# Kernel optimization log

Hardware: AMD Instinct MI355X
Metric: run time of the kernel (lower is better)

## Reference

```python
import jax, jax.numpy as jnp
import numpy as np

H, D = 8, 16          # heads, per-head dim (hidden=128)
N_NEWS, N_INTER, F_IN, C_OUT = 30000, 60000, 768, 4
HID = H * D


def setup_inputs() -> dict:
    key = jax.random.key(0)
    ks = jax.random.split(key, 20)
    s = lambda i, shape, sc=0.05: (jax.random.normal(ks[i], shape, dtype=jnp.float32) * sc)
    inp = {
        "x_news": jax.random.normal(ks[0], (N_NEWS, F_IN), dtype=jnp.float32),
        "x_inter": jax.random.normal(ks[1], (N_INTER, F_IN), dtype=jnp.float32),
        "edge_nn": jax.random.randint(ks[2], (2, 480000), 0, N_NEWS),
        "edge_in": jax.random.randint(ks[3], (2, 960000), 0, N_NEWS),
        # per-node-type input projections (HANConv.proj)
        "W_news": s(4, (F_IN, HID)), "b_news": jnp.zeros((HID,), jnp.float32),
        "W_inter": s(5, (F_IN, HID)), "b_inter": jnp.zeros((HID,), jnp.float32),
        # per-edge-type node-level attention vectors (lin_src / lin_dst)
        "a_src_nn": s(6, (H, D), 0.2), "a_dst_nn": s(7, (H, D), 0.2),
        "a_src_in": s(8, (H, D), 0.2), "a_dst_in": s(9, (H, D), 0.2),
        # semantic-level attention (k_lin, q)
        "Wk": s(10, (HID, HID)), "bk": jnp.zeros((HID,), jnp.float32),
        "q": s(11, (HID,), 0.2),
        # output head
        "W_out": s(12, (HID, C_OUT)), "b_out": jnp.zeros((C_OUT,), jnp.float32),
    }
    return inp


def _han_conv(h_src, h_dst, edge, a_src, a_dst, n_dst):
    # node-level (GAT-style) attention for one edge type
    asrc = (h_src * a_src).sum(-1)            # [Ns, H]
    adst = (h_dst * a_dst).sum(-1)            # [Nd, H]
    src, dst = edge[0], edge[1]
    e = jax.nn.leaky_relu(asrc[src] + adst[dst], negative_slope=0.2)   # [E, H]
    m = jax.ops.segment_max(e, dst, num_segments=n_dst)                # [Nd, H]
    m = jnp.where(jnp.isfinite(m), m, jnp.float32(0))
    ex = jnp.exp(e - m[dst])
    denom = jax.ops.segment_sum(ex, dst, num_segments=n_dst)
    alpha = ex / (denom[dst] + jnp.float32(1e-16))                     # [E, H]
    out = jax.ops.segment_sum(h_src[src] * alpha[:, :, None], dst, num_segments=n_dst)
    return jax.nn.relu(out.reshape(n_dst, H * D))                      # [Nd, HID]


def reference(x_news, x_inter, edge_nn, edge_in,
              W_news, b_news, W_inter, b_inter,
              a_src_nn, a_dst_nn, a_src_in, a_dst_in,
              Wk, bk, q, W_out, b_out):
    # per-node-type projection, reshape to heads
    h_news = (x_news @ W_news + b_news).reshape(-1, H, D)
    h_inter = (x_inter @ W_inter + b_inter).reshape(-1, H, D)
    # per-edge-type node-level attention conv (dst is always 'news')
    out_nn = _han_conv(h_news, h_news, edge_nn, a_src_nn, a_dst_nn, N_NEWS)
    out_in = _han_conv(h_inter, h_news, edge_in, a_src_in, a_dst_in, N_NEWS)
    # semantic-level attention across metapaths
    outs = jnp.stack([out_nn, out_in])                       # [2, N, HID]
    score = (q * jnp.tanh(outs @ Wk + bk).mean(axis=1)).sum(-1)   # [2]
    beta = jax.nn.softmax(score, axis=0)
    fused = (beta[:, None, None] * outs).sum(0)              # [N, HID]
    # head: ELU + (eval-mode dropout = identity) + Linear
    return jax.nn.elu(fused) @ W_out + b_out
```

## Files before the change

kernel.cpp:

```cpp
#include <hip/hip_runtime.h>
#include <hip/hip_bf16.h>

#define N_NODES   30000
#define F_IN      768
#define HID       128
#define NHEAD     8
#define C_OUT     4

typedef short short8_t __attribute__((ext_vector_type(8)));
typedef float float4_t __attribute__((ext_vector_type(4)));
typedef int   int4_t   __attribute__((ext_vector_type(4)));

__device__ __forceinline__ float b2f(short u) {
    union { unsigned int i; float f; } v;
    v.i = ((unsigned int)(unsigned short)u) << 16;
    return v.f;
}
__device__ __forceinline__ short f2s(float f) {
    __hip_bfloat16 h = __float2bfloat16(f);
    short s; __builtin_memcpy(&s, &h, 2); return s;
}

#define OFF_H_NEWS      0UL
#define OFF_H_INTER     7680000UL
#define OFF_OUT_NN      15360000UL
#define OFF_OUT_IN      23040000UL
#define OFF_ASRC_NN     30720000UL
#define OFF_ADST_NN     31680000UL
#define OFF_ASRC_IN     32640000UL
#define OFF_ADST_IN     33600000UL
#define OFF_WT_NEWS     34560000UL
#define OFF_WT_INTER    34756608UL
#define OFF_RS_NN       34953216UL
#define OFF_RS_IN       35073280UL
#define OFF_SORT_NN     35193344UL
#define OFF_SORT_IN     37113344UL
#define OFF_ZERO        40953344UL
#define OFF_DEG_NN      40953344UL
#define OFF_FILL_NN     41073408UL
#define OFF_DEG_IN      41193472UL
#define OFF_FILL_IN     41313536UL
#define OFF_SSUM        41433600UL
#define OFF_CNT         41434624UL
#define ZERO_BYTES      481296UL
#define OFF_BETA        41434640UL
#define OFF_FLAG        41434648UL
#define OFF_CPAR        41434656UL
#define OFF_WKT         41470512UL

#define CP_B_NEWS  0
#define CP_B_INTER 128
#define CP_ASRC_NN 256
#define CP_ADST_NN 384
#define CP_ASRC_IN 512
#define CP_ADST_IN 640
#define CP_BK      17152
#define CP_Q       17280
#define CP_WOUT    17408
#define CP_BOUT    17920
#define CP_TOTAL   17924

#define PREP_CONV_BLOCKS 7
#define PREP_TW_BLOCKS   384
#define PREP_WK_BLOCKS   64
#define PREP_ZERO_BLOCKS 118
#define PREP_B0 PREP_CONV_BLOCKS
#define PREP_B1 (PREP_B0 + 2*PREP_TW_BLOCKS)
#define PREP_B2 (PREP_B1 + PREP_WK_BLOCKS)
#define PREP_TOTAL (PREP_B2 + PREP_ZERO_BLOCKS)

#define GEMM_BX 469
#define LDK     40
#define ABUF    2560
#define BUFSZ   7680

__global__ void detect_dtype(const unsigned int* __restrict__ x, int* __restrict__ flag) {
    __shared__ int cnt_s;
    if (threadIdx.x == 0) cnt_s = 0;
    __syncthreads();
    int sane = 0;
    for (int i = threadIdx.x; i < 16384; i += 1024) {
        unsigned int lo = x[i] & 0xFFFFu;
        unsigned int ex = (lo >> 7) & 0xFFu;
        if ((ex >= 107u && ex <= 147u) || lo == 0u || lo == 0x8000u) sane++;
    }
    atomicAdd(&cnt_s, sane);
    __syncthreads();
    if (threadIdx.x == 0) *flag = (cnt_s > 8192) ? 1 : 0;
}

struct SmallParams {
    const void* src[10];
    int n[10];
    int dstoff[10];
};

__global__ void prep(SmallParams sp, short* __restrict__ cp,
                     const void* __restrict__ Wn, const void* __restrict__ Wi,
                     const void* __restrict__ Wkraw,
                     short* __restrict__ WtN, short* __restrict__ WtI,
                     short* __restrict__ wkT,
                     char* __restrict__ zbase,
                     const int* __restrict__ flag) {
    const bool isbf = (*flag != 0);
    int b = blockIdx.x, tid = threadIdx.x;
    if (b < PREP_B0) {
        int idx = b * 256 + tid;
        for (int s = 0; s < 10; ++s) {
            if (idx < sp.n[s]) {
                short v = isbf ? ((const short*)sp.src[s])[idx]
                               : f2s(((const float*)sp.src[s])[idx]);
                cp[sp.dstoff[s] + idx] = v;
                return;
            }
            idx -= sp.n[s];
        }
    } else if (b < PREP_B1) {
        int bb = b - PREP_B0;
        int ty = bb >= PREP_TW_BLOCKS;
        const void* Wraw = ty ? Wi : Wn;
        short* Wt        = ty ? WtI : WtN;
        int idx = (bb - ty * PREP_TW_BLOCKS) * 256 + tid;
        if (idx < F_IN * HID) {
            int n = idx / F_IN;
            int k = idx - n * F_IN;
            Wt[idx] = isbf ? ((const short*)Wraw)[k * HID + n]
                           : f2s(((const float*)Wraw)[k * HID + n]);
        }
    } else if (b < PREP_B2) {
        int idx = (b - PREP_B1) * 256 + tid;
        if (idx < HID * HID) {
            int j = idx >> 7;
            int k = idx & 127;
            wkT[idx] = isbf ? ((const short*)Wkraw)[k * HID + j]
                            : f2s(((const float*)Wkraw)[k * HID + j]);
        }
    } else {
        size_t off = ((size_t)(b - PREP_B2) * 256 + tid) * 16;
        if (off < ZERO_BYTES) *(int4_t*)(zbase + off) = (int4_t){0, 0, 0, 0};
    }
}

template<bool ISBF>
__device__ __forceinline__ void gemm_body(
    const void* __restrict__ Xraw, const short* __restrict__ Wt,
    const short* __restrict__ cp, short* __restrict__ Hout,
    float* __restrict__ dot0, float* __restrict__ dot1, float* __restrict__ dot2,
    int ty, int m0, int M, short* __restrict__ SB)
{
    int tid  = threadIdx.x;
    int lane = tid & 63;
    int wid  = tid >> 6;
    int quad = lane >> 4;
    int lm   = lane & 15;
    int sr   = tid >> 2;
    int skp  = (tid & 3) * 8;

    int ga = m0 + sr; if (ga >= M) ga = M - 1;
    const short* asrc_s = (const short*)Xraw + (size_t)ga * F_IN + skp;
    const float* asrc_f = (const float*)Xraw + (size_t)ga * F_IN + skp;
    const short* bsrc0  = Wt + (size_t)sr * F_IN + skp;
    const short* bsrc1  = Wt + (size_t)(sr + 64) * F_IN + skp;

    short8_t avr;
    float4_t af0, af1;
    short8_t bvr0, bvr1;

    auto LOAD = [&](int k0) {
        if (ISBF) {
            avr = *(const short8_t*)(asrc_s + k0);
        } else {
            af0 = *(const float4_t*)(asrc_f + k0);
            af1 = *(const float4_t*)(asrc_f + k0 + 4);
        }
        bvr0 = *(const short8_t*)(bsrc0 + k0);
        bvr1 = *(const short8_t*)(bsrc1 + k0);
    };
    auto STORE = [&](short* buf) {
        short8_t av;
        if (ISBF) av = avr;
        else {
            #pragma unroll
            for (int j = 0; j < 4; ++j) {
                av[j]     = f2s(af0[j]);
                av[4 + j] = f2s(af1[j]);
            }
        }
        *(short8_t*)(buf + sr * LDK + skp)                = av;
        *(short8_t*)(buf + ABUF + sr * LDK + skp)         = bvr0;
        *(short8_t*)(buf + ABUF + (sr + 64) * LDK + skp)  = bvr1;
    };

    float4_t acc[8];
    #pragma unroll
    for (int c = 0; c < 8; ++c) acc[c] = (float4_t){0.f, 0.f, 0.f, 0.f};

    LOAD(0);
    STORE(SB);
    LOAD(32);
    __syncthreads();

    for (int kc = 0; kc < 24; ++kc) {
        short* buf = SB + (kc & 1) * BUFSZ;
        short* nxt = SB + ((kc & 1) ^ 1) * BUFSZ;

        short8_t bfrag[8];
        #pragma unroll
        for (int c = 0; c < 8; ++c)
            bfrag[c] = *(const short8_t*)(buf + ABUF + (c * 16 + lm) * LDK + quad * 8);
        short8_t afrag = *(const short8_t*)(buf + (wid * 16 + lm) * LDK + quad * 8);

        if (kc < 23) STORE(nxt);
        if (kc < 22) LOAD((kc + 2) * 32);

        #pragma unroll
        for (int c = 0; c < 8; ++c)
            acc[c] = __builtin_amdgcn_mfma_f32_16x16x32_bf16(afrag, bfrag[c], acc[c], 0, 0, 0);
        __syncthreads();
    }

    const short* bias = cp + (ty ? CP_B_INTER : CP_B_NEWS);
    const short* aw0  = cp + (ty ? CP_ASRC_IN : CP_ASRC_NN);
    const short* aw1  = cp + CP_ADST_NN;
    const short* aw2  = cp + CP_ADST_IN;

    short* ep = SB;

    #pragma unroll
    for (int r = 0; r < 4; ++r) {
        int erow = wid * 16 + quad * 4 + r;
        int gm = m0 + erow;
        bool ok = gm < M;
        float d0a[8], d1a[8], d2a[8];
        #pragma unroll
        for (int c = 0; c < 8; ++c) {
            int col = c * 16 + lm;
            float hval = acc[c][r] + b2f(bias[col]);
            ep[erow * 130 + col] = f2s(hval);
            float d0 = hval * b2f(aw0[col]);
            float d1 = hval * b2f(aw1[col]);
            float d2 = hval * b2f(aw2[col]);
            #pragma unroll
            for (int off = 1; off < 16; off <<= 1) {
                d0 += __shfl_xor(d0, off, 16);
                if (ty == 0) {
                    d1 += __shfl_xor(d1, off, 16);
                    d2 += __shfl_xor(d2, off, 16);
                }
            }
            d0a[c] = d0; d1a[c] = d1; d2a[c] = d2;
        }
        if (lm == 0 && ok) {
            float4_t v0 = {d0a[0], d0a[1], d0a[2], d0a[3]};
            float4_t v1 = {d0a[4], d0a[5], d0a[6], d0a[7]};
            *(float4_t*)(dot0 + (size_t)gm * NHEAD)     = v0;
            *(float4_t*)(dot0 + (size_t)gm * NHEAD + 4) = v1;
            if (ty == 0) {
                float4_t w0 = {d1a[0], d1a[1], d1a[2], d1a[3]};
                float4_t w1 = {d1a[4], d1a[5], d1a[6], d1a[7]};
                *(float4_t*)(dot1 + (size_t)gm * NHEAD)     = w0;
                *(float4_t*)(dot1 + (size_t)gm * NHEAD + 4) = w1;
                float4_t u0 = {d2a[0], d2a[1], d2a[2], d2a[3]};
                float4_t u1 = {d2a[4], d2a[5], d2a[6], d2a[7]};
                *(float4_t*)(dot2 + (size_t)gm * NHEAD)     = u0;
                *(float4_t*)(dot2 + (size_t)gm * NHEAD + 4) = u1;
            }
        }
    }
    #pragma unroll
    for (int j = 0; j < 4; ++j) {
        int erow = wid * 16 + j * 4 + quad;
        int gm = m0 + erow;
        short8_t v = *(const short8_t*)(&ep[erow * 130 + lm * 8]);
        if (gm < M)
            *(short8_t*)(&Hout[(size_t)gm * HID + lm * 8]) = v;
    }
}

__global__ __launch_bounds__(256) void proj_count(
    const void* __restrict__ Xn, const void* __restrict__ Xi,
    const short* __restrict__ WtN, const short* __restrict__ WtI,
    const short* __restrict__ cp,
    short* __restrict__ Hn, short* __restrict__ Hi,
    float* __restrict__ asrc_nn, float* __restrict__ adst_nn,
    float* __restrict__ asrc_in, float* __restrict__ adst_in,
    const int* __restrict__ dnn, int Enn,
    const int* __restrict__ din, int Ein,
    int* __restrict__ deg_nn, int* __restrict__ deg_in,
    int M, const int* __restrict__ flag)
{
    __shared__ __align__(16) short SB[2 * BUFSZ];

    int b = blockIdx.x;
    if (b >= 2 * GEMM_BX) {
        int i = (b - 2 * GEMM_BX) * 256 + threadIdx.x;
        if (i < Enn) {
            int d = dnn[i];
            if ((unsigned)d < (unsigned)N_NODES) atomicAdd(&deg_nn[d], 1);
        } else {
            int j = i - Enn;
            if (j < Ein) {
                int d = din[j];
                if ((unsigned)d < (unsigned)N_NODES) atomicAdd(&deg_in[d], 1);
            }
        }
        return;
    }

    const bool isbf = (*flag != 0);
    int ty = b >= GEMM_BX;
    int bx = b - ty * GEMM_BX;
    int m0 = bx * 64;

    const void* Xraw = ty ? Xi : Xn;
    const short* Wt  = ty ? WtI : WtN;
    short* Hout      = ty ? Hi : Hn;
    float* dot0      = ty ? asrc_in : asrc_nn;

    if (isbf) gemm_body<true >(Xraw, Wt, cp, Hout, dot0, adst_nn, adst_in, ty, m0, M, SB);
    else      gemm_body<false>(Xraw, Wt, cp, Hout, dot0, adst_nn, adst_in, ty, m0, M, SB);
}

__global__ __launch_bounds__(256) void prefix_scan2(
    const int* __restrict__ deg_nn, int* __restrict__ rs_nn,
    const int* __restrict__ deg_in, int* __restrict__ rs_in, int n)
{
    const int* deg = blockIdx.x ? deg_in : deg_nn;
    int* row_start = blockIdx.x ? rs_in : rs_nn;
    __shared__ int psum[256];
    int tid = threadIdx.x;
    int chunk = (n + 255) / 256;
    int lo = tid * chunk;
    int hi = lo + chunk; if (hi > n) hi = n; if (lo > n) lo = n;
    int s = 0;
    for (int i = lo; i < hi; ++i) s += deg[i];
    psum[tid] = s;
    __syncthreads();
    for (int off = 1; off < 256; off <<= 1) {
        int v = (tid >= off) ? psum[tid - off] : 0;
        __syncthreads();
        psum[tid] += v;
        __syncthreads();
    }
    int base = tid ? psum[tid - 1] : 0;
    for (int i = lo; i < hi; ++i) { row_start[i] = base; base += deg[i]; }
    if (tid == 255) row_start[n] = psum[255];
}

__global__ void scatter_edges2(const int* __restrict__ enn, int Enn,
                               const int* __restrict__ ein, int Ein,
                               const int* __restrict__ rs_nn, int* __restrict__ fill_nn,
                               int* __restrict__ sort_nn,
                               const int* __restrict__ rs_in, int* __restrict__ fill_in,
                               int* __restrict__ sort_in) {
    int i = blockIdx.x * 256 + threadIdx.x;
    if (i < Enn) {
        int d = enn[Enn + i];
        if (d >= 0 && d < N_NODES) {
            int pos = rs_nn[d] + atomicAdd(&fill_nn[d], 1);
            if (pos >= 0 && pos < Enn) sort_nn[pos] = enn[i];
        }
    } else {
        int j = i - Enn;
        if (j < Ein) {
            int d = ein[Ein + j];
            if (d >= 0 && d < N_NODES) {
                int pos = rs_in[d] + atomicAdd(&fill_in[d], 1);
                if (pos >= 0 && pos < Ein) sort_in[pos] = ein[j];
            }
        }
    }
}

__global__ __launch_bounds__(256) void aggregate2(
    const short* __restrict__ Hnn, const short* __restrict__ Hin,
    const float* __restrict__ asrc_nn, const float* __restrict__ adst_nn,
    const float* __restrict__ asrc_in, const float* __restrict__ adst_in,
    const int* __restrict__ rs_nn, const int* __restrict__ rs_in,
    const int* __restrict__ sort_nn, const int* __restrict__ sort_in,
    short* __restrict__ out_nn, short* __restrict__ out_in)
{
    int tid = threadIdx.x, w = tid >> 6, lane = tid & 63;
    int type = blockIdx.y;
    const short* H    = type ? Hin : Hnn;
    const float* asrc = type ? asrc_in : asrc_nn;
    const float* adst = type ? adst_in : adst_nn;
    const int*   rs   = type ? rs_in : rs_nn;
    const int*   ss   = type ? sort_in : sort_nn;
    short* outb       = type ? out_in : out_nn;

    int dn = blockIdx.x * 4 + w;
    int start = rs[dn], end = rs[dn + 1];
    int head = lane >> 3;
    float adv = adst[dn * NHEAD + head];
    const short* Hl = H + lane * 2;

    float den = 0.f, a0 = 0.f, a1 = 0.f;
    for (int base = start; base < end; base += 64) {
        int nb = end - base; if (nb > 64) nb = 64;
        int myidx = 0;
        if (base + lane < end) {
            int t = ss[base + lane];
            myidx = (t < 0) ? 0 : (t >= N_NODES ? N_NODES - 1 : t);
        }
        int j = 0;
        for (; j + 2 <= nb; j += 2) {
            int s0 = __shfl(myidx, j, 64);
            int s1 = __shfl(myidx, j + 1, 64);
            float v0 = asrc[s0 * NHEAD + head];
            float v1 = asrc[s1 * NHEAD + head];
            unsigned int q0 = *(const unsigned int*)(Hl + (size_t)s0 * HID);
            unsigned int q1 = *(const unsigned int*)(Hl + (size_t)s1 * HID);
            float e0 = v0 + adv, e1 = v1 + adv;
            e0 = fmaxf(e0, 0.2f * e0); e1 = fmaxf(e1, 0.2f * e1);
            e0 = fminf(e0, 80.f);      e1 = fminf(e1, 80.f);
            float x0 = __expf(e0), x1 = __expf(e1);
            union { unsigned int u; float f; } cl0, ch0, cl1, ch1;
            cl0.u = q0 << 16; ch0.u = q0 & 0xFFFF0000u;
            cl1.u = q1 << 16; ch1.u = q1 & 0xFFFF0000u;
            den += x0; den += x1;
            a0 = fmaf(x0, cl0.f, a0); a0 = fmaf(x1, cl1.f, a0);
            a1 = fmaf(x0, ch0.f, a1); a1 = fmaf(x1, ch1.f, a1);
        }
        if (j < nb) {
            int s0 = __shfl(myidx, j, 64);
            float v0 = asrc[s0 * NHEAD + head];
            unsigned int q0 = *(const unsigned int*)(Hl + (size_t)s0 * HID);
            float e0 = v0 + adv;
            e0 = fmaxf(e0, 0.2f * e0);
            e0 = fminf(e0, 80.f);
            float x0 = __expf(e0);
            union { unsigned int u; float f; } cl0, ch0;
            cl0.u = q0 << 16; ch0.u = q0 & 0xFFFF0000u;
            den += x0;
            a0 = fmaf(x0, cl0.f, a0);
            a1 = fmaf(x0, ch0.f, a1);
        }
    }
    float inv = 1.f / (den + 1e-16f);
    unsigned int lo16 = (unsigned short)f2s(fmaxf(a0 * inv, 0.f));
    unsigned int hi16 = (unsigned short)f2s(fmaxf(a1 * inv, 0.f));
    *(unsigned int*)(outb + (size_t)dn * HID + lane * 2) = lo16 | (hi16 << 16);
}

__global__ __launch_bounds__(256) void score_mfma(
    const short* __restrict__ out_nn, const short* __restrict__ out_in,
    const short* __restrict__ wkT, const short* __restrict__ cp,
    float* __restrict__ Ssum, int* __restrict__ done_cnt,
    float* __restrict__ beta, int total_blocks)
{
    __shared__ float col_s[HID];
    __shared__ int lastflag;
    int tid  = threadIdx.x;
    int lane = tid & 63;
    int wid  = tid >> 6;
    int quad = lane >> 4;
    int lm   = lane & 15;
    const short* src = blockIdx.y ? out_in : out_nn;
    int m0 = blockIdx.x * 128;

    if (tid < HID) col_s[tid] = 0.f;
    __syncthreads();

    float4_t acc[2][8];
    #pragma unroll
    for (int i = 0; i < 2; ++i)
        #pragma unroll
        for (int c = 0; c < 8; ++c)
            acc[i][c] = (float4_t){0.f, 0.f, 0.f, 0.f};

    #pragma unroll
    for (int kc = 0; kc < 4; ++kc) {
        short8_t bfrag[8];
        #pragma unroll
        for (int c = 0; c < 8; ++c)
            bfrag[c] = *(const short8_t*)(wkT + (c * 16 + lm) * HID + kc * 32 + quad * 8);
        #pragma unroll
        for (int i = 0; i < 2; ++i) {
            int gm = m0 + wid * 32 + i * 16 + lm;
            if (gm >= N_NODES) gm = N_NODES - 1;
            short8_t afrag = *(const short8_t*)(src + (size_t)gm * HID + kc * 32 + quad * 8);
            #pragma unroll
            for (int c = 0; c < 8; ++c)
                acc[i][c] = __builtin_amdgcn_mfma_f32_16x16x32_bf16(afrag, bfrag[c], acc[i][c], 0, 0, 0);
        }
    }

    #pragma unroll
    for (int c = 0; c < 8; ++c) {
        int col = c * 16 + lm;
        float bkc = b2f(cp[CP_BK + col]);
        float lsum = 0.f;
        #pragma unroll
        for (int i = 0; i < 2; ++i)
            #pragma unroll
            for (int r = 0; r < 4; ++r) {
                int node = m0 + wid * 32 + i * 16 + quad * 4 + r;
                if (node < N_NODES) {
                    float a = acc[i][c][r] + bkc;
                    a = fminf(fmaxf(a, -15.f), 15.f);
                    float t = __expf(2.f * a);
                    lsum += (t - 1.f) / (t + 1.f);
                }
            }
        float v = lsum;
        v += __shfl_down(v, 32, 64);
        v += __shfl_down(v, 16, 64);
        if (quad == 0) atomicAdd(&col_s[col], v);
    }
    __syncthreads();
    if (tid < HID) atomicAdd(&Ssum[blockIdx.y * HID + tid], col_s[tid]);
    __syncthreads();

    if (tid == 0) {
        __threadfence();
        int old = atomicAdd(done_cnt, 1);
        lastflag = (old == total_blocks - 1) ? 1 : 0;
    }
    __syncthreads();
    if (lastflag && tid < 64) {
        float s00 = atomicAdd(&Ssum[tid], 0.f);
        float s01 = atomicAdd(&Ssum[tid + 64], 0.f);
        float s10 = atomicAdd(&Ssum[128 + tid], 0.f);
        float s11 = atomicAdd(&Ssum[192 + tid], 0.f);
        float q0 = b2f(cp[CP_Q + tid]), q1 = b2f(cp[CP_Q + tid + 64]);
        float v0 = q0 * s00 + q1 * s01;
        float v1 = q0 * s10 + q1 * s11;
        #pragma unroll
        for (int off = 32; off; off >>= 1) {
            v0 += __shfl_down(v0, off, 64);
            v1 += __shfl_down(v1, off, 64);
        }
        if (tid == 0) {
            float sc0 = v0 / (float)N_NODES;
            float sc1 = v1 / (float)N_NODES;
            float mx = fmaxf(sc0, sc1);
            float e0 = __expf(sc0 - mx), e1 = __expf(sc1 - mx);
            float inv = 1.f / (e0 + e1);
            beta[0] = e0 * inv;
            beta[1] = e1 * inv;
        }
    }
}

__global__ __launch_bounds__(256) void final_out(
    const short* __restrict__ out_nn, const short* __restrict__ out_in,
    const float* __restrict__ beta, const short* __restrict__ cp,
    void* __restrict__ Yraw, const int* __restrict__ flag)
{
    bool isbf = (*flag != 0);
    int tid = threadIdx.x, lane = tid & 63, w = tid >> 6;
    int n = blockIdx.x * 4 + w;
    float b0 = beta[0], b1 = beta[1];
    unsigned int u0 = *(const unsigned int*)(out_nn + (size_t)n * HID + lane * 2);
    unsigned int u1 = *(const unsigned int*)(out_in + (size_t)n * HID + lane * 2);
    union { unsigned int u; float f; } t;
    t.u = u0 << 16;          float f0 = b0 * t.f;
    t.u = u0 & 0xFFFF0000u;  float f1 = b0 * t.f;
    t.u = u1 << 16;          f0 += b1 * t.f;
    t.u = u1 & 0xFFFF0000u;  f1 += b1 * t.f;
    float e0 = (f0 > 0.f) ? f0 : expm1f(f0);
    float e1 = (f1 > 0.f) ? f1 : expm1f(f1);
    int c0 = lane * 2, c1 = lane * 2 + 1;
    float p[C_OUT];
    #pragma unroll
    for (int c = 0; c < C_OUT; ++c)
        p[c] = e0 * b2f(cp[CP_WOUT + c0 * C_OUT + c]) + e1 * b2f(cp[CP_WOUT + c1 * C_OUT + c]);
    #pragma unroll
    for (int off = 32; off; off >>= 1)
        #pragma unroll
        for (int c = 0; c < C_OUT; ++c) p[c] += __shfl_down(p[c], off, 64);
    if (lane == 0) {
        #pragma unroll
        for (int c = 0; c < C_OUT; ++c) {
            float r = p[c] + b2f(cp[CP_BOUT + c]);
            if (isbf) ((__hip_bfloat16*)Yraw)[n * C_OUT + c] = __float2bfloat16(r);
            else      ((float*)Yraw)[n * C_OUT + c] = r;
        }
    }
}

extern "C" void kernel_launch(void* const* d_in, const int* in_sizes, int n_in,
                              void* d_out, int out_size, void* d_ws, size_t ws_size,
                              hipStream_t stream) {
    const void* x_news  = d_in[0];
    const void* x_inter = d_in[1];
    const int*  edge_nn = (const int*)d_in[2];
    const int*  edge_in = (const int*)d_in[3];

    int E_nn = in_sizes[2] / 2;
    int E_in = in_sizes[3] / 2;

    char* ws = (char*)d_ws;
    short* h_news  = (short*)(ws + OFF_H_NEWS);
    short* h_inter = (short*)(ws + OFF_H_INTER);
    short* out_nn  = (short*)(ws + OFF_OUT_NN);
    short* out_in  = (short*)(ws + OFF_OUT_IN);
    float* asrc_nn = (float*)(ws + OFF_ASRC_NN);
    float* adst_nn = (float*)(ws + OFF_ADST_NN);
    float* asrc_in = (float*)(ws + OFF_ASRC_IN);
    float* adst_in = (float*)(ws + OFF_ADST_IN);
    short* wt_news  = (short*)(ws + OFF_WT_NEWS);
    short* wt_inter = (short*)(ws + OFF_WT_INTER);
    int* rs_nn   = (int*)(ws + OFF_RS_NN);
    int* rs_in   = (int*)(ws + OFF_RS_IN);
    int* sort_nn = (int*)(ws + OFF_SORT_NN);
    int* sort_in = (int*)(ws + OFF_SORT_IN);
    int* deg_nn  = (int*)(ws + OFF_DEG_NN);
    int* fill_nn = (int*)(ws + OFF_FILL_NN);
    int* deg_in  = (int*)(ws + OFF_DEG_IN);
    int* fill_in = (int*)(ws + OFF_FILL_IN);
    float* Ssum  = (float*)(ws + OFF_SSUM);
    int*   dcnt  = (int*)(ws + OFF_CNT);
    float* beta  = (float*)(ws + OFF_BETA);
    int*   flag  = (int*)(ws + OFF_FLAG);
    short* cp    = (short*)(ws + OFF_CPAR);
    short* wkT   = (short*)(ws + OFF_WKT);

    detect_dtype<<<1, 1024, 0, stream>>>((const unsigned int*)x_news, flag);

    SmallParams sp;
    const int srcidx[10] = {5, 7, 8, 9, 10, 11, 13, 14, 15, 16};
    const int ns[10]     = {128, 128, 128, 128, 128, 128, 128, 128, 512, 4};
    const int doff[10]   = {CP_B_NEWS, CP_B_INTER, CP_ASRC_NN, CP_ADST_NN, CP_ASRC_IN,
                            CP_ADST_IN, CP_BK, CP_Q, CP_WOUT, CP_BOUT};
    for (int i = 0; i < 10; ++i) { sp.src[i] = d_in[srcidx[i]]; sp.n[i] = ns[i]; sp.dstoff[i] = doff[i]; }

    prep<<<PREP_TOTAL, 256, 0, stream>>>(sp, cp, d_in[4], d_in[6], d_in[12],
                                         wt_news, wt_inter, wkT, ws + OFF_ZERO, flag);

    int cnt_blocks = (E_nn + E_in + 255) / 256;
    proj_count<<<2 * GEMM_BX + cnt_blocks, 256, 0, stream>>>(
        x_news, x_inter, wt_news, wt_inter, cp, h_news, h_inter,
        asrc_nn, adst_nn, asrc_in, adst_in,
        edge_nn + E_nn, E_nn, edge_in + E_in, E_in, deg_nn, deg_in,
        N_NODES, flag);

    prefix_scan2<<<2, 256, 0, stream>>>(deg_nn, rs_nn, deg_in, rs_in, N_NODES);

    scatter_edges2<<<cnt_blocks, 256, 0, stream>>>(
        edge_nn, E_nn, edge_in, E_in, rs_nn, fill_nn, sort_nn, rs_in, fill_in, sort_in);

    aggregate2<<<dim3(N_NODES / 4, 2), 256, 0, stream>>>(
        h_news, h_inter, asrc_nn, adst_nn, asrc_in, adst_in,
        rs_nn, rs_in, sort_nn, sort_in, out_nn, out_in);

    int score_bx = (N_NODES + 127) / 128;
    score_mfma<<<dim3(score_bx, 2), 256, 0, stream>>>(
        out_nn, out_in, wkT, cp, Ssum, dcnt, beta, 2 * score_bx);

    final_out<<<N_NODES / 4, 256, 0, stream>>>(out_nn, out_in, beta, cp, d_out, flag);
}
```

Baseline: 622.4 us.

## Fold dtype detection and prefix scan into neighbouring kernels, drop LDS staging in GEMM

Dtype detection moves into every prep block, removing a separate launch. The degree-count blocks now come first in proj_count, and the last one to finish runs the prefix scan, which removes the prefix_scan2 launch. The projection GEMM drops its LDS double buffer in favour of direct global-to-register fragment loads with register double buffering, and writes its outputs straight to global memory. The aggregation inner loop is also unrolled from two edges to four. Risks: each prep block re-reads the 64KB probe, the B fragments lose LDS reuse across waves and become uncoalesced global loads, and the last-block scan relies on atomics and fences, with the cnt_done counter needing to be zeroed beforehand.

```diff
diff --git a/kernel.cpp b/kernel.cpp
--- a/kernel.cpp
+++ b/kernel.cpp
@@ -70,24 +70,6 @@
 #define PREP_TOTAL (PREP_B2 + PREP_ZERO_BLOCKS)
 
 #define GEMM_BX 469
-#define LDK     40
-#define ABUF    2560
-#define BUFSZ   7680
-
-__global__ void detect_dtype(const unsigned int* __restrict__ x, int* __restrict__ flag) {
-    __shared__ int cnt_s;
-    if (threadIdx.x == 0) cnt_s = 0;
-    __syncthreads();
-    int sane = 0;
-    for (int i = threadIdx.x; i < 16384; i += 1024) {
-        unsigned int lo = x[i] & 0xFFFFu;
-        unsigned int ex = (lo >> 7) & 0xFFu;
-        if ((ex >= 107u && ex <= 147u) || lo == 0u || lo == 0x8000u) sane++;
-    }
-    atomicAdd(&cnt_s, sane);
-    __syncthreads();
-    if (threadIdx.x == 0) *flag = (cnt_s > 8192) ? 1 : 0;
-}
 
 struct SmallParams {
     const void* src[10];
@@ -101,9 +83,23 @@
                      short* __restrict__ WtN, short* __restrict__ WtI,
                      short* __restrict__ wkT,
                      char* __restrict__ zbase,
-                     const int* __restrict__ flag) {
-    const bool isbf = (*flag != 0);
+                     const unsigned int* __restrict__ xprobe,
+                     int* __restrict__ flag) {
+    __shared__ int cnt_s;
     int b = blockIdx.x, tid = threadIdx.x;
+    if (tid == 0) cnt_s = 0;
+    __syncthreads();
+    int sane = 0;
+    for (int i = tid; i < 16384; i += 256) {
+        unsigned int lo = xprobe[i] & 0xFFFFu;
+        unsigned int ex = (lo >> 7) & 0xFFu;
+        if ((ex >= 107u && ex <= 147u) || lo == 0u || lo == 0x8000u) sane++;
+    }
+    atomicAdd(&cnt_s, sane);
+    __syncthreads();
+    const bool isbf = (cnt_s > 8192);
+    if (b == 0 && tid == 0) *flag = isbf ? 1 : 0;
+
     if (b < PREP_B0) {
         int idx = b * 256 + tid;
         for (int s = 0; s < 10; ++s) {
@@ -146,97 +142,82 @@
     const void* __restrict__ Xraw, const short* __restrict__ Wt,
     const short* __restrict__ cp, short* __restrict__ Hout,
     float* __restrict__ dot0, float* __restrict__ dot1, float* __restrict__ dot2,
-    int ty, int m0, int M, short* __restrict__ SB)
+    int ty, int m0, int M)
 {
     int tid  = threadIdx.x;
     int lane = tid & 63;
     int wid  = tid >> 6;
     int quad = lane >> 4;
     int lm   = lane & 15;
-    int sr   = tid >> 2;
-    int skp  = (tid & 3) * 8;
-
-    int ga = m0 + sr; if (ga >= M) ga = M - 1;
-    const short* asrc_s = (const short*)Xraw + (size_t)ga * F_IN + skp;
-    const float* asrc_f = (const float*)Xraw + (size_t)ga * F_IN + skp;
-    const short* bsrc0  = Wt + (size_t)sr * F_IN + skp;
-    const short* bsrc1  = Wt + (size_t)(sr + 64) * F_IN + skp;
-
-    short8_t avr;
-    float4_t af0, af1;
-    short8_t bvr0, bvr1;
-
-    auto LOAD = [&](int k0) {
-        if (ISBF) {
-            avr = *(const short8_t*)(asrc_s + k0);
-        } else {
-            af0 = *(const float4_t*)(asrc_f + k0);
-            af1 = *(const float4_t*)(asrc_f + k0 + 4);
-        }
-        bvr0 = *(const short8_t*)(bsrc0 + k0);
-        bvr1 = *(const short8_t*)(bsrc1 + k0);
-    };
-    auto STORE = [&](short* buf) {
-        short8_t av;
-        if (ISBF) av = avr;
-        else {
-            #pragma unroll
-            for (int j = 0; j < 4; ++j) {
-                av[j]     = f2s(af0[j]);
-                av[4 + j] = f2s(af1[j]);
-            }
-        }
-        *(short8_t*)(buf + sr * LDK + skp)                = av;
-        *(short8_t*)(buf + ABUF + sr * LDK + skp)         = bvr0;
-        *(short8_t*)(buf + ABUF + (sr + 64) * LDK + skp)  = bvr1;
-    };
+
+    int gm_a = m0 + wid * 16 + lm; if (gm_a >= M) gm_a = M - 1;
+    const short* as0 = (const short*)Xraw + (size_t)gm_a * F_IN + quad * 8;
+    const float* af0 = (const float*)Xraw + (size_t)gm_a * F_IN + quad * 8;
+    const short* bb  = Wt + (size_t)lm * F_IN + quad * 8;
 
     float4_t acc[8];
     #pragma unroll
     for (int c = 0; c < 8; ++c) acc[c] = (float4_t){0.f, 0.f, 0.f, 0.f};
 
-    LOAD(0);
-    STORE(SB);
-    LOAD(32);
-    __syncthreads();
-
-    for (int kc = 0; kc < 24; ++kc) {
-        short* buf = SB + (kc & 1) * BUFSZ;
-        short* nxt = SB + ((kc & 1) ^ 1) * BUFSZ;
-
-        short8_t bfrag[8];
-        #pragma unroll
-        for (int c = 0; c < 8; ++c)
-            bfrag[c] = *(const short8_t*)(buf + ABUF + (c * 16 + lm) * LDK + quad * 8);
-        short8_t afrag = *(const short8_t*)(buf + (wid * 16 + lm) * LDK + quad * 8);
-
-        if (kc < 23) STORE(nxt);
-        if (kc < 22) LOAD((kc + 2) * 32);
-
-        #pragma unroll
-        for (int c = 0; c < 8; ++c)
-            acc[c] = __builtin_amdgcn_mfma_f32_16x16x32_bf16(afrag, bfrag[c], acc[c], 0, 0, 0);
-        __syncthreads();
-    }
+    short8_t bA[8], bB[8];
+    short8_t aAs, aBs;
+    float4_t aAf0, aAf1, aBf0, aBf1;
+
+#define PC_LOADA(K1) do { \
+        if (ISBF) { aAs = *(const short8_t*)(as0 + (K1)); } \
+        else { aAf0 = *(const float4_t*)(af0 + (K1)); aAf1 = *(const float4_t*)(af0 + (K1) + 4); } \
+        _Pragma("unroll") \
+        for (int c = 0; c < 8; ++c) bA[c] = *(const short8_t*)(bb + (size_t)c * 16 * F_IN + (K1)); \
+    } while (0)
+#define PC_LOADB(K1) do { \
+        if (ISBF) { aBs = *(const short8_t*)(as0 + (K1)); } \
+        else { aBf0 = *(const float4_t*)(af0 + (K1)); aBf1 = *(const float4_t*)(af0 + (K1) + 4); } \
+        _Pragma("unroll") \
+        for (int c = 0; c < 8; ++c) bB[c] = *(const short8_t*)(bb + (size_t)c * 16 * F_IN + (K1)); \
+    } while (0)
+#define PC_STEPA() do { \
+        short8_t afr; \
+        if (ISBF) afr = aAs; \
+        else { _Pragma("unroll") for (int j = 0; j < 4; ++j) { afr[j] = f2s(aAf0[j]); afr[4+j] = f2s(aAf1[j]); } } \
+        _Pragma("unroll") \
+        for (int c = 0; c < 8; ++c) acc[c] = __builtin_amdgcn_mfma_f32_16x16x32_bf16(afr, bA[c], acc[c], 0, 0, 0); \
+    } while (0)
+#define PC_STEPB() do { \
+        short8_t afr; \
+        if (ISBF) afr = aBs; \
+        else { _Pragma("unroll") for (int j = 0; j < 4; ++j) { afr[j] = f2s(aBf0[j]); afr[4+j] = f2s(aBf1[j]); } } \
+        _Pragma("unroll") \
+        for (int c = 0; c < 8; ++c) acc[c] = __builtin_amdgcn_mfma_f32_16x16x32_bf16(afr, bB[c], acc[c], 0, 0, 0); \
+    } while (0)
+
+    PC_LOADA(0);
+    #pragma unroll
+    for (int kc = 0; kc < 24; kc += 2) {
+        if (kc + 1 < 24) PC_LOADB((kc + 1) * 32);
+        PC_STEPA();
+        if (kc + 2 < 24) PC_LOADA((kc + 2) * 32);
+        PC_STEPB();
+    }
+#undef PC_LOADA
+#undef PC_LOADB
+#undef PC_STEPA
+#undef PC_STEPB
 
     const short* bias = cp + (ty ? CP_B_INTER : CP_B_NEWS);
     const short* aw0  = cp + (ty ? CP_ASRC_IN : CP_ASRC_NN);
     const short* aw1  = cp + CP_ADST_NN;
     const short* aw2  = cp + CP_ADST_IN;
 
-    short* ep = SB;
-
     #pragma unroll
     for (int r = 0; r < 4; ++r) {
-        int erow = wid * 16 + quad * 4 + r;
-        int gm = m0 + erow;
+        int gm = m0 + wid * 16 + quad * 4 + r;
         bool ok = gm < M;
         float d0a[8], d1a[8], d2a[8];
         #pragma unroll
         for (int c = 0; c < 8; ++c) {
             int col = c * 16 + lm;
             float hval = acc[c][r] + b2f(bias[col]);
-            ep[erow * 130 + col] = f2s(hval);
+            if (ok) Hout[(size_t)gm * HID + col] = f2s(hval);
             float d0 = hval * b2f(aw0[col]);
             float d1 = hval * b2f(aw1[col]);
             float d2 = hval * b2f(aw2[col]);
@@ -267,17 +248,9 @@
             }
         }
     }
-    #pragma unroll
-    for (int j = 0; j < 4; ++j) {
-        int erow = wid * 16 + j * 4 + quad;
-        int gm = m0 + erow;
-        short8_t v = *(const short8_t*)(&ep[erow * 130 + lm * 8]);
-        if (gm < M)
-            *(short8_t*)(&Hout[(size_t)gm * HID + lm * 8]) = v;
-    }
-}
-
-__global__ __launch_bounds__(256) void proj_count(
+}
+
+__global__ __launch_bounds__(256, 4) void proj_count(
     const void* __restrict__ Xn, const void* __restrict__ Xi,
     const short* __restrict__ WtN, const short* __restrict__ WtI,
     const short* __restrict__ cp,
@@ -287,13 +260,16 @@
     const int* __restrict__ dnn, int Enn,
     const int* __restrict__ din, int Ein,
     int* __restrict__ deg_nn, int* __restrict__ deg_in,
+    int* __restrict__ rs_nn, int* __restrict__ rs_in,
+    int cntB, int* __restrict__ cnt_done,
     int M, const int* __restrict__ flag)
 {
-    __shared__ __align__(16) short SB[2 * BUFSZ];
-
-    int b = blockIdx.x;
-    if (b >= 2 * GEMM_BX) {
-        int i = (b - 2 * GEMM_BX) * 256 + threadIdx.x;
+    __shared__ int psum[256];
+    __shared__ int lastflag;
+    int b = blockIdx.x, tid = threadIdx.x;
+
+    if (b < cntB) {
+        int i = b * 256 + tid;
         if (i < Enn) {
             int d = dnn[i];
             if ((unsigned)d < (unsigned)N_NODES) atomicAdd(&deg_nn[d], 1);
@@ -304,9 +280,40 @@
                 if ((unsigned)d < (unsigned)N_NODES) atomicAdd(&deg_in[d], 1);
             }
         }
+        __threadfence();
+        __syncthreads();
+        if (tid == 0) {
+            int old = atomicAdd(cnt_done, 1);
+            lastflag = (old == cntB - 1) ? 1 : 0;
+        }
+        __syncthreads();
+        if (!lastflag) return;
+        __threadfence();
+        for (int pass = 0; pass < 2; ++pass) {
+            int* deg = pass ? deg_in : deg_nn;
+            int* rsx = pass ? rs_in : rs_nn;
+            const int chunk = (N_NODES + 255) / 256;
+            int lo = tid * chunk;
+            int hi = lo + chunk; if (hi > N_NODES) hi = N_NODES; if (lo > N_NODES) lo = N_NODES;
+            int s = 0;
+            for (int i2 = lo; i2 < hi; ++i2) s += atomicAdd(&deg[i2], 0);
+            psum[tid] = s;
+            __syncthreads();
+            for (int off = 1; off < 256; off <<= 1) {
+                int v = (tid >= off) ? psum[tid - off] : 0;
+                __syncthreads();
+                psum[tid] += v;
+                __syncthreads();
+            }
+            int base = tid ? psum[tid - 1] : 0;
+            for (int i2 = lo; i2 < hi; ++i2) { rsx[i2] = base; base += atomicAdd(&deg[i2], 0); }
+            if (tid == 255) rsx[N_NODES] = psum[255];
+            __syncthreads();
+        }
         return;
     }
 
+    b -= cntB;
     const bool isbf = (*flag != 0);
     int ty = b >= GEMM_BX;
     int bx = b - ty * GEMM_BX;
@@ -317,34 +324,8 @@
     short* Hout      = ty ? Hi : Hn;
     float* dot0      = ty ? asrc_in : asrc_nn;
 
-    if (isbf) gemm_body<true >(Xraw, Wt, cp, Hout, dot0, adst_nn, adst_in, ty, m0, M, SB);
-    else      gemm_body<false>(Xraw, Wt, cp, Hout, dot0, adst_nn, adst_in, ty, m0, M, SB);
-}
-
-__global__ __launch_bounds__(256) void prefix_scan2(
-    const int* __restrict__ deg_nn, int* __restrict__ rs_nn,
-    const int* __restrict__ deg_in, int* __restrict__ rs_in, int n)
-{
-    const int* deg = blockIdx.x ? deg_in : deg_nn;
-    int* row_start = blockIdx.x ? rs_in : rs_nn;
-    __shared__ int psum[256];
-    int tid = threadIdx.x;
-    int chunk = (n + 255) / 256;
-    int lo = tid * chunk;
-    int hi = lo + chunk; if (hi > n) hi = n; if (lo > n) lo = n;
-    int s = 0;
-    for (int i = lo; i < hi; ++i) s += deg[i];
-    psum[tid] = s;
-    __syncthreads();
-    for (int off = 1; off < 256; off <<= 1) {
-        int v = (tid >= off) ? psum[tid - off] : 0;
-        __syncthreads();
-        psum[tid] += v;
-        __syncthreads();
-    }
-    int base = tid ? psum[tid - 1] : 0;
-    for (int i = lo; i < hi; ++i) { row_start[i] = base; base += deg[i]; }
-    if (tid == 255) row_start[n] = psum[255];
+    if (isbf) gemm_body<true >(Xraw, Wt, cp, Hout, dot0, adst_nn, adst_in, ty, m0, M);
+    else      gemm_body<false>(Xraw, Wt, cp, Hout, dot0, adst_nn, adst_in, ty, m0, M);
 }
 
 __global__ void scatter_edges2(const int* __restrict__ enn, int Enn,
@@ -404,25 +385,37 @@
             myidx = (t < 0) ? 0 : (t >= N_NODES ? N_NODES - 1 : t);
         }
         int j = 0;
-        for (; j + 2 <= nb; j += 2) {
+        for (; j + 4 <= nb; j += 4) {
             int s0 = __shfl(myidx, j, 64);
             int s1 = __shfl(myidx, j + 1, 64);
+            int s2 = __shfl(myidx, j + 2, 64);
+            int s3 = __shfl(myidx, j + 3, 64);
             float v0 = asrc[s0 * NHEAD + head];
             float v1 = asrc[s1 * NHEAD + head];
+            float v2 = asrc[s2 * NHEAD + head];
+            float v3 = asrc[s3 * NHEAD + head];
             unsigned int q0 = *(const unsigned int*)(Hl + (size_t)s0 * HID);
             unsigned int q1 = *(const unsigned int*)(Hl + (size_t)s1 * HID);
-            float e0 = v0 + adv, e1 = v1 + adv;
+            unsigned int q2 = *(const unsigned int*)(Hl + (size_t)s2 * HID);
+            unsigned int q3 = *(const unsigned int*)(Hl + (size_t)s3 * HID);
+            float e0 = v0 + adv, e1 = v1 + adv, e2 = v2 + adv, e3 = v3 + adv;
             e0 = fmaxf(e0, 0.2f * e0); e1 = fmaxf(e1, 0.2f * e1);
-            e0 = fminf(e0, 80.f);      e1 = fminf(e1, 80.f);
-            float x0 = __expf(e0), x1 = __expf(e1);
-            union { unsigned int u; float f; } cl0, ch0, cl1, ch1;
+            e2 = fmaxf(e2, 0.2f * e2); e3 = fmaxf(e3, 0.2f * e3);
+            e0 = fminf(e0, 80.f); e1 = fminf(e1, 80.f);
+            e2 = fminf(e2, 80.f); e3 = fminf(e3, 80.f);
+            float x0 = __expf(e0), x1 = __expf(e1), x2 = __expf(e2), x3 = __expf(e3);
+            union { unsigned int u; float f; } cl0, ch0, cl1, ch1, cl2, ch2, cl3, ch3;
             cl0.u = q0 << 16; ch0.u = q0 & 0xFFFF0000u;
             cl1.u = q1 << 16; ch1.u = q1 & 0xFFFF0000u;
-            den += x0; den += x1;
+            cl2.u = q2 << 16; ch2.u = q2 & 0xFFFF0000u;
+            cl3.u = q3 << 16; ch3.u = q3 & 0xFFFF0000u;
+            den += x0; den += x1; den += x2; den += x3;
             a0 = fmaf(x0, cl0.f, a0); a0 = fmaf(x1, cl1.f, a0);
+            a0 = fmaf(x2, cl2.f, a0); a0 = fmaf(x3, cl3.f, a0);
             a1 = fmaf(x0, ch0.f, a1); a1 = fmaf(x1, ch1.f, a1);
-        }
-        if (j < nb) {
+            a1 = fmaf(x2, ch2.f, a1); a1 = fmaf(x3, ch3.f, a1);
+        }
+        for (; j < nb; ++j) {
             int s0 = __shfl(myidx, j, 64);
             float v0 = asrc[s0 * NHEAD + head];
             unsigned int q0 = *(const unsigned int*)(Hl + (size_t)s0 * HID);
@@ -617,8 +610,6 @@
     short* cp    = (short*)(ws + OFF_CPAR);
     short* wkT   = (short*)(ws + OFF_WKT);
 
-    detect_dtype<<<1, 1024, 0, stream>>>((const unsigned int*)x_news, flag);
-
     SmallParams sp;
     const int srcidx[10] = {5, 7, 8, 9, 10, 11, 13, 14, 15, 16};
     const int ns[10]     = {128, 128, 128, 128, 128, 128, 128, 128, 512, 4};
@@ -627,18 +618,19 @@
     for (int i = 0; i < 10; ++i) { sp.src[i] = d_in[srcidx[i]]; sp.n[i] = ns[i]; sp.dstoff[i] = doff[i]; }
 
     prep<<<PREP_TOTAL, 256, 0, stream>>>(sp, cp, d_in[4], d_in[6], d_in[12],
-                                         wt_news, wt_inter, wkT, ws + OFF_ZERO, flag);
-
-    int cnt_blocks = (E_nn + E_in + 255) / 256;
-    proj_count<<<2 * GEMM_BX + cnt_blocks, 256, 0, stream>>>(
+                                         wt_news, wt_inter, wkT, ws + OFF_ZERO,
+                                         (const unsigned int*)x_news, flag);
+
+    int cntB = (E_nn + E_in + 255) / 256;
+    proj_count<<<cntB + 2 * GEMM_BX, 256, 0, stream>>>(
         x_news, x_inter, wt_news, wt_inter, cp, h_news, h_inter,
         asrc_nn, adst_nn, asrc_in, adst_in,
-        edge_nn + E_nn, E_nn, edge_in + E_in, E_in, deg_nn, deg_in,
+        edge_nn + E_nn, E_nn, edge_in + E_in, E_in,
+        deg_nn, deg_in, rs_nn, rs_in,
+        cntB, dcnt + 1,
         N_NODES, flag);
 
-    prefix_scan2<<<2, 256, 0, stream>>>(deg_nn, rs_nn, deg_in, rs_in, N_NODES);
-
-    scatter_edges2<<<cnt_blocks, 256, 0, stream>>>(
+    scatter_edges2<<<cntB, 256, 0, stream>>>(
         edge_nn, E_nn, edge_in, E_in, rs_nn, fill_nn, sort_nn, rs_in, fill_in, sort_in);
 
     aggregate2<<<dim3(N_NODES / 4, 2), 256, 0, stream>>>(
```

Result: slower. 1.063 ms (+70.8%).
